# Kernel tuning notes

Hardware: AMD Instinct MI355X
Metric: run time of the kernel (lower is better)

The kernel has to match this reference:

```python
import jax, jax.numpy as jnp
import numpy as np

L = 2          # MPblock_layers
H = 64         # hidden_channels
B, N, E = 1, 50000, 800000


def setup_inputs() -> dict:
    key = jax.random.key(0)
    ks = jax.random.split(key, 12)
    s = 0.05
    return {
        "x": jax.random.normal(ks[0], (B, N, H), jnp.float32),
        "edge_attr": jax.random.normal(ks[1], (B, E, H), jnp.float32),
        "edge_index": jax.random.randint(ks[2], (2, E), 0, N, jnp.int64 if jax.config.jax_enable_x64 else jnp.int32),
        # per-layer stacked MLP params: edge MLP (3H->H->H), node MLP (2H->H->H)
        "edge_w1": jax.random.normal(ks[3], (L, 3 * H, H), jnp.float32) * s,
        "edge_b1": jnp.zeros((L, H), jnp.float32),
        "edge_w2": jax.random.normal(ks[4], (L, H, H), jnp.float32) * s,
        "edge_b2": jnp.zeros((L, H), jnp.float32),
        "node_w1": jax.random.normal(ks[5], (L, 2 * H, H), jnp.float32) * s,
        "node_b1": jnp.zeros((L, H), jnp.float32),
        "node_w2": jax.random.normal(ks[6], (L, H, H), jnp.float32) * s,
        "node_b2": jnp.zeros((L, H), jnp.float32),
    }


def reference(x, edge_attr, edge_index,
              edge_w1, edge_b1, edge_w2, edge_b2,
              node_w1, node_b1, node_w2, node_b2):
    src = edge_index[0]
    dest = edge_index[1]
    n_nodes = x.shape[1]
    for l in range(L):
        # EdgeModel: cat([edge_attr, x[src], x[dest]]) -> MLP
        cat_e = jnp.concatenate([edge_attr, x[:, src], x[:, dest]], axis=2)  # [B,E,3H]
        h = jax.nn.silu(jnp.einsum('bef,fh->beh', cat_e, edge_w1[l]) + edge_b1[l])
        edge_attr = jnp.einsum('beh,hk->bek', h, edge_w2[l]) + edge_b2[l]      # [B,E,H]
        # NodeModel: scatter_add over dest, cat with x, MLP
        agg = jnp.zeros((x.shape[0], n_nodes, edge_attr.shape[2]), x.dtype).at[:, dest].add(edge_attr)
        cat_n = jnp.concatenate([x, agg], axis=2)                              # [B,N,2H]
        h = jax.nn.silu(jnp.einsum('bnf,fh->bnh', cat_n, node_w1[l]) + node_b1[l])
        x = jnp.einsum('bnh,hk->bnk', h, node_w2[l]) + node_b2[l]              # [B,N,H]
    return (x, edge_attr)
```

## Files before the change

### kernel.cpp

```cpp
#include <hip/hip_runtime.h>

typedef __attribute__((ext_vector_type(8))) _Float16 f16x8;
typedef __attribute__((ext_vector_type(4))) _Float16 f16x4;
typedef __attribute__((ext_vector_type(4))) float f32x4;

#define PWS 72

__device__ __forceinline__ float silu_f(float v) {
    return v * (1.0f / (1.0f + __expf(-v)));
}

struct WDesc { const float* W; _Float16* out; int K; };
struct WPack { WDesc d[8]; };

__global__ __launch_bounds__(256) void conv_weights(WPack p) {
    WDesc wd = p.d[blockIdx.y];
    int total = wd.K * 64;
    int i = blockIdx.x * 256 + threadIdx.x;
    if (i >= total) return;
    int j  = i & 7;
    int l  = (i >> 3) & 63;
    int tn = i >> 9;
    int t  = tn >> 2, nf = tn & 3;
    int k  = t * 32 + (l >> 4) * 8 + j;
    int c  = nf * 16 + (l & 15);
    wd.out[i] = (_Float16)wd.W[k * 64 + c];
}

template <bool IN16, bool OUT16>
__global__ __launch_bounds__(256, 8) void gnn_edge_mfma(
    const float* __restrict__ x,
    const float* __restrict__ ea_in,
    const _Float16* __restrict__ ea_in16,
    float* __restrict__ ea_out,
    _Float16* __restrict__ ea_out16,
    const int* __restrict__ src_idx,
    const int* __restrict__ dst_idx,
    const _Float16* __restrict__ w1f,
    const float* __restrict__ b1,
    const _Float16* __restrict__ w2f,
    const float* __restrict__ b2,
    float* __restrict__ agg,
    int E)
{
    __shared__ __align__(16) _Float16 sA[64][PWS];

    const int t    = threadIdx.x;
    const int lane = t & 63;
    const int w    = t >> 6;
    const int col  = lane & 15;
    const int g    = lane >> 4;
    const int ko   = g * 8;
    const long base = (long)blockIdx.x * 64;

    long er0 = base + w * 16 + col;
    if (er0 >= E) er0 = E - 1;
    const int di = dst_idx[er0];

    f16x4  ea16v[4];
    float4 ea4[4];
    float4 sx4[4], dx4[4];
#pragma unroll
    for (int it = 0; it < 4; ++it) {
        long er = base + w * 16 + it * 4 + g;
        if (er >= E) er = E - 1;
        if constexpr (IN16) ea16v[it] = *(const f16x4*)(ea_in16 + er * 64 + col * 4);
        else                ea4[it]   = *(const float4*)(ea_in   + er * 64 + col * 4);
        sx4[it] = *(const float4*)(x + (long)src_idx[er] * 64 + col * 4);
        dx4[it] = *(const float4*)(x + (long)dst_idx[er] * 64 + col * 4);
    }

    f32x4 acc[4];
#pragma unroll
    for (int nf = 0; nf < 4; ++nf) {
        float bv = b1[nf * 16 + col];
        acc[nf] = (f32x4){bv, bv, bv, bv};
    }

    const int arow = w * 16 + col;

#define MFMA_L1(s3)                                                             \
    _Pragma("unroll")                                                           \
    for (int tt = 0; tt < 2; ++tt) {                                            \
        int k0 = tt * 32 + ko;                                                  \
        f16x8 af = *(const f16x8*)&sA[arow][k0];                                \
        int tg = (s3) * 2 + tt;                                                 \
        _Pragma("unroll")                                                       \
        for (int nf = 0; nf < 4; ++nf) {                                        \
            f16x8 bf = *(const f16x8*)(w1f + (size_t)((tg*4+nf)*64+lane)*8);    \
            acc[nf] = __builtin_amdgcn_mfma_f32_16x16x32_f16(af, bf, acc[nf], 0, 0, 0); \
        }                                                                       \
    }

#pragma unroll
    for (int it = 0; it < 4; ++it) {
        int rg = w * 16 + it * 4 + g;
        f16x4 hv;
        if constexpr (IN16) {
            hv = ea16v[it];
        } else {
            hv[0] = (_Float16)ea4[it].x; hv[1] = (_Float16)ea4[it].y;
            hv[2] = (_Float16)ea4[it].z; hv[3] = (_Float16)ea4[it].w;
        }
        *(f16x4*)&sA[rg][col * 4] = hv;
    }
    MFMA_L1(0)

#pragma unroll
    for (int it = 0; it < 4; ++it) {
        int rg = w * 16 + it * 4 + g;
        f16x4 hv;
        hv[0] = (_Float16)sx4[it].x; hv[1] = (_Float16)sx4[it].y;
        hv[2] = (_Float16)sx4[it].z; hv[3] = (_Float16)sx4[it].w;
        *(f16x4*)&sA[rg][col * 4] = hv;
    }
    MFMA_L1(1)

#pragma unroll
    for (int it = 0; it < 4; ++it) {
        int rg = w * 16 + it * 4 + g;
        f16x4 hv;
        hv[0] = (_Float16)dx4[it].x; hv[1] = (_Float16)dx4[it].y;
        hv[2] = (_Float16)dx4[it].z; hv[3] = (_Float16)dx4[it].w;
        *(f16x4*)&sA[rg][col * 4] = hv;
    }
    MFMA_L1(2)
#undef MFMA_L1

#pragma unroll
    for (int nf = 0; nf < 4; ++nf)
#pragma unroll
        for (int rg = 0; rg < 4; ++rg) {
            int row = w * 16 + g * 4 + rg;
            sA[row][nf * 16 + col] = (_Float16)silu_f(acc[nf][rg]);
        }

    f32x4 out[4];
#pragma unroll
    for (int nf = 0; nf < 4; ++nf) {
        float bv = b2[nf * 16 + col];
        out[nf] = (f32x4){bv, bv, bv, bv};
    }
#pragma unroll
    for (int tt = 0; tt < 2; ++tt) {
        int k0 = tt * 32 + ko;
        f16x8 af = *(const f16x8*)&sA[arow][k0];
#pragma unroll
        for (int nf = 0; nf < 4; ++nf) {
            f16x8 bf = *(const f16x8*)(w2f + (size_t)((tt * 4 + nf) * 64 + lane) * 8);
            out[nf] = __builtin_amdgcn_mfma_f32_16x16x32_f16(af, bf, out[nf], 0, 0, 0);
        }
    }

    const int rbase = w * 16 + g * 4;
#pragma unroll
    for (int rg = 0; rg < 4; ++rg) {
        long row = base + rbase + rg;
        if (row < E) {
            int drow = __shfl(di, g * 4 + rg);
            float* ap = agg + (long)drow * 64;
#pragma unroll
            for (int nf = 0; nf < 4; ++nf) {
                if constexpr (OUT16)
                    ea_out16[row * 64 + nf * 16 + col] = (_Float16)out[nf][rg];
                else
                    ea_out[row * 64 + nf * 16 + col] = out[nf][rg];
                atomicAdd(&ap[nf * 16 + col], out[nf][rg]);
            }
        }
    }
}

__global__ __launch_bounds__(256, 8) void gnn_node_mfma(
    const float* __restrict__ x_in,
    const float* __restrict__ aggp,
    float* __restrict__ x_out,
    const _Float16* __restrict__ w1f,
    const float* __restrict__ b1,
    const _Float16* __restrict__ w2f,
    const float* __restrict__ b2, int N)
{
    __shared__ __align__(16) _Float16 sA[64][PWS];

    const int t    = threadIdx.x;
    const int lane = t & 63;
    const int w    = t >> 6;
    const int col  = lane & 15;
    const int g    = lane >> 4;
    const int ko   = g * 8;
    const long base = (long)blockIdx.x * 64;

    long nr = base + w * 16 + col;
    if (nr >= N) nr = N - 1;
    const float* px = x_in + nr * 64 + ko;
    const float* pa = aggp + nr * 64 + ko;

    float4 v0 = *(const float4*)(px);
    float4 v1 = *(const float4*)(px + 4);
    float4 v2 = *(const float4*)(px + 32);
    float4 v3 = *(const float4*)(px + 36);
    float4 v4 = *(const float4*)(pa);
    float4 v5 = *(const float4*)(pa + 4);
    float4 v6 = *(const float4*)(pa + 32);
    float4 v7 = *(const float4*)(pa + 36);

    f32x4 acc[4];
#pragma unroll
    for (int nf = 0; nf < 4; ++nf) {
        float bv = b1[nf * 16 + col];
        acc[nf] = (f32x4){bv, bv, bv, bv};
    }

#define QTR(m, A, B)                                                            \
    {                                                                           \
        f16x8 af;                                                               \
        af[0] = (_Float16)A.x; af[1] = (_Float16)A.y;                           \
        af[2] = (_Float16)A.z; af[3] = (_Float16)A.w;                           \
        af[4] = (_Float16)B.x; af[5] = (_Float16)B.y;                           \
        af[6] = (_Float16)B.z; af[7] = (_Float16)B.w;                           \
        _Pragma("unroll")                                                       \
        for (int nf = 0; nf < 4; ++nf) {                                        \
            f16x8 bf = *(const f16x8*)(w1f + (size_t)(((m)*4+nf)*64+lane)*8);   \
            acc[nf] = __builtin_amdgcn_mfma_f32_16x16x32_f16(af, bf, acc[nf], 0, 0, 0); \
        }                                                                       \
    }
    QTR(0, v0, v1)  QTR(1, v2, v3)
    QTR(2, v4, v5)  QTR(3, v6, v7)
#undef QTR

#pragma unroll
    for (int nf = 0; nf < 4; ++nf)
#pragma unroll
        for (int rg = 0; rg < 4; ++rg) {
            int row = w * 16 + g * 4 + rg;
            sA[row][nf * 16 + col] = (_Float16)silu_f(acc[nf][rg]);
        }

    f32x4 out[4];
#pragma unroll
    for (int nf = 0; nf < 4; ++nf) {
        float bv = b2[nf * 16 + col];
        out[nf] = (f32x4){bv, bv, bv, bv};
    }
    const int arow = w * 16 + col;
#pragma unroll
    for (int tt = 0; tt < 2; ++tt) {
        int k0 = tt * 32 + ko;
        f16x8 af = *(const f16x8*)&sA[arow][k0];
#pragma unroll
        for (int nf = 0; nf < 4; ++nf) {
            f16x8 bf = *(const f16x8*)(w2f + (size_t)((tt * 4 + nf) * 64 + lane) * 8);
            out[nf] = __builtin_amdgcn_mfma_f32_16x16x32_f16(af, bf, out[nf], 0, 0, 0);
        }
    }

    const int rbase = w * 16 + g * 4;
#pragma unroll
    for (int rg = 0; rg < 4; ++rg) {
        long row = base + rbase + rg;
        if (row < N) {
            float* op = x_out + row * 64;
#pragma unroll
            for (int nf = 0; nf < 4; ++nf)
                op[nf * 16 + col] = out[nf][rg];
        }
    }
}

extern "C" void kernel_launch(void* const* d_in, const int* in_sizes, int n_in,
                              void* d_out, int out_size, void* d_ws, size_t ws_size,
                              hipStream_t stream) {
    const int H = 64;
    const int N = in_sizes[0] / H;
    const int E = in_sizes[1] / H;

    const float* x0  = (const float*)d_in[0];
    const float* ea0 = (const float*)d_in[1];
    const int*   ei  = (const int*)d_in[2];
    const float* ew1 = (const float*)d_in[3];
    const float* eb1 = (const float*)d_in[4];
    const float* ew2 = (const float*)d_in[5];
    const float* eb2 = (const float*)d_in[6];
    const float* nw1 = (const float*)d_in[7];
    const float* nb1 = (const float*)d_in[8];
    const float* nw2 = (const float*)d_in[9];
    const float* nb2 = (const float*)d_in[10];

    float* outX = (float*)d_out;
    float* outE = outX + (size_t)N * H;

    const size_t aggBytes = (size_t)N * H * sizeof(float);
    const size_t wElems   = 2 * ((size_t)(192 + 64 + 128 + 64) * 64);
    const size_t eaHBytes = (size_t)E * H * sizeof(_Float16);

    float* agg      = (float*)d_ws;
    _Float16* wbase = (_Float16*)((char*)d_ws + aggBytes);
    char* eaH_raw   = (char*)(wbase + wElems);
    eaH_raw = (char*)(((uintptr_t)eaH_raw + 15) & ~(uintptr_t)15);
    _Float16* eaH   = (_Float16*)eaH_raw;

    const bool useF16 = ((char*)eaH + eaHBytes) <= ((char*)d_ws + ws_size);

    const int* srcI = ei;
    const int* dstI = ei + E;

    WPack pack;
    size_t off = 0;
    _Float16* EW1[2]; _Float16* EW2[2]; _Float16* NW1[2]; _Float16* NW2[2];
    for (int l = 0; l < 2; ++l) {
        EW1[l] = wbase + off; off += 192 * 64;
        EW2[l] = wbase + off; off += 64 * 64;
        NW1[l] = wbase + off; off += 128 * 64;
        NW2[l] = wbase + off; off += 64 * 64;
        pack.d[l * 4 + 0] = {ew1 + (size_t)l * 192 * 64, EW1[l], 192};
        pack.d[l * 4 + 1] = {ew2 + (size_t)l * 64 * 64,  EW2[l], 64};
        pack.d[l * 4 + 2] = {nw1 + (size_t)l * 128 * 64, NW1[l], 128};
        pack.d[l * 4 + 3] = {nw2 + (size_t)l * 64 * 64,  NW2[l], 64};
    }
    conv_weights<<<dim3(48, 8), 256, 0, stream>>>(pack);

    const int egrid = (E + 63) / 64;
    const int ngrid = (N + 63) / 64;

    for (int l = 0; l < 2; ++l) {
        const float* xin = (l == 0) ? x0 : outX;
        (void)hipMemsetAsync(agg, 0, aggBytes, stream);
        if (useF16) {
            if (l == 0) {
                gnn_edge_mfma<false, true><<<egrid, 256, 0, stream>>>(
                    xin, ea0, nullptr, nullptr, eaH, srcI, dstI,
                    EW1[l], eb1 + l * H, EW2[l], eb2 + l * H, agg, E);
            } else {
                gnn_edge_mfma<true, false><<<egrid, 256, 0, stream>>>(
                    xin, nullptr, eaH, outE, nullptr, srcI, dstI,
                    EW1[l], eb1 + l * H, EW2[l], eb2 + l * H, agg, E);
            }
        } else {
            const float* eain = (l == 0) ? ea0 : outE;
            gnn_edge_mfma<false, false><<<egrid, 256, 0, stream>>>(
                xin, eain, nullptr, outE, nullptr, srcI, dstI,
                EW1[l], eb1 + l * H, EW2[l], eb2 + l * H, agg, E);
        }
        gnn_node_mfma<<<ngrid, 256, 0, stream>>>(
            xin, agg, outX,
            NW1[l], nb1 + l * H,
            NW2[l], nb2 + l * H,
            N);
    }
}
```

Baseline: 540.3 us.

## Sort edges by destination into CSR and replace atomic scatter with segmented reduction

Builds a destination-sorted CSR each call (histogram, single-block scan, atomic scatter) and runs the edge MLP in sorted order, writing fp16 edge outputs contiguously. A per-node segmented-sum kernel then replaces the float atomic scatter-add and the agg memset. The final layer also scatters fp32 results back to the original edge order. This adds sorting kernels, a serial 1024-thread scan and extra index traffic, and the edge_attr gather in layer one becomes a permuted read.

```diff
diff --git a/kernel.cpp b/kernel.cpp
--- a/kernel.cpp
+++ b/kernel.cpp
@@ -25,6 +25,223 @@
     int k  = t * 32 + (l >> 4) * 8 + j;
     int c  = nf * 16 + (l & 15);
     wd.out[i] = (_Float16)wd.W[k * 64 + c];
+}
+
+__global__ __launch_bounds__(256) void hist_kernel(const int* __restrict__ dst,
+                                                   int* __restrict__ counts, int E) {
+    int e = blockIdx.x * 256 + threadIdx.x;
+    if (e < E) atomicAdd(&counts[dst[e]], 1);
+}
+
+__global__ __launch_bounds__(1024) void scan_kernel(int* __restrict__ counts,
+                                                    int* __restrict__ row_ptr,
+                                                    int N, int E) {
+    __shared__ int part[1024];
+    int t = threadIdx.x;
+    int per = (N + 1023) >> 10;
+    int s = t * per, en = min(s + per, N);
+    int sum = 0;
+    for (int i = s; i < en; ++i) sum += counts[i];
+    part[t] = sum;
+    __syncthreads();
+    for (int off = 1; off < 1024; off <<= 1) {
+        int v = (t >= off) ? part[t - off] : 0;
+        __syncthreads();
+        part[t] += v;
+        __syncthreads();
+    }
+    int run = (t == 0) ? 0 : part[t - 1];
+    for (int i = s; i < en; ++i) {
+        int c = counts[i];
+        row_ptr[i] = run;
+        counts[i] = run;
+        run += c;
+    }
+    if (t == 1023) row_ptr[N] = E;
+}
+
+__global__ __launch_bounds__(256) void scatter_kernel(
+    const int* __restrict__ src, const int* __restrict__ dst,
+    int* __restrict__ cursor,
+    int* __restrict__ csr_eid, int* __restrict__ srcS, int* __restrict__ dstS,
+    int E) {
+    int e = blockIdx.x * 256 + threadIdx.x;
+    if (e < E) {
+        int d = dst[e];
+        int pos = atomicAdd(&cursor[d], 1);
+        csr_eid[pos] = e;
+        srcS[pos] = src[e];
+        dstS[pos] = d;
+    }
+}
+
+template <bool IN16, bool FINAL>
+__global__ __launch_bounds__(256, 8) void gnn_edge_sorted(
+    const float* __restrict__ x,
+    const float* __restrict__ ea0,
+    _Float16* __restrict__ ea_mid,
+    float* __restrict__ ea_out,
+    const int* __restrict__ csr_eid,
+    const int* __restrict__ srcS,
+    const int* __restrict__ dstS,
+    const _Float16* __restrict__ w1f,
+    const float* __restrict__ b1,
+    const _Float16* __restrict__ w2f,
+    const float* __restrict__ b2,
+    int E)
+{
+    __shared__ __align__(16) _Float16 sA[64][PWS];
+
+    const int t    = threadIdx.x;
+    const int lane = t & 63;
+    const int w    = t >> 6;
+    const int col  = lane & 15;
+    const int g    = lane >> 4;
+    const int ko   = g * 8;
+    const long base = (long)blockIdx.x * 64;
+
+    long p0 = base + w * 16 + col;
+    if (p0 >= E) p0 = E - 1;
+    int ei0 = 0;
+    if constexpr (FINAL) ei0 = csr_eid[p0];
+
+    f16x4  ea16v[4];
+    float4 ea4[4];
+    float4 sx4[4], dx4[4];
+#pragma unroll
+    for (int it = 0; it < 4; ++it) {
+        long p = base + w * 16 + it * 4 + g;
+        if (p >= E) p = E - 1;
+        int ss = srcS[p];
+        int ds = dstS[p];
+        if constexpr (IN16) {
+            ea16v[it] = *(const f16x4*)(ea_mid + p * 64 + col * 4);
+        } else {
+            int eid = csr_eid[p];
+            ea4[it] = *(const float4*)(ea0 + (long)eid * 64 + col * 4);
+        }
+        sx4[it] = *(const float4*)(x + (long)ss * 64 + col * 4);
+        dx4[it] = *(const float4*)(x + (long)ds * 64 + col * 4);
+    }
+
+    f32x4 acc[4];
+#pragma unroll
+    for (int nf = 0; nf < 4; ++nf) {
+        float bv = b1[nf * 16 + col];
+        acc[nf] = (f32x4){bv, bv, bv, bv};
+    }
+
+    const int arow = w * 16 + col;
+
+#define MFMA_L1(s3)                                                             \
+    _Pragma("unroll")                                                           \
+    for (int tt = 0; tt < 2; ++tt) {                                            \
+        int k0 = tt * 32 + ko;                                                  \
+        f16x8 af = *(const f16x8*)&sA[arow][k0];                                \
+        int tg = (s3) * 2 + tt;                                                 \
+        _Pragma("unroll")                                                       \
+        for (int nf = 0; nf < 4; ++nf) {                                        \
+            f16x8 bf = *(const f16x8*)(w1f + (size_t)((tg*4+nf)*64+lane)*8);    \
+            acc[nf] = __builtin_amdgcn_mfma_f32_16x16x32_f16(af, bf, acc[nf], 0, 0, 0); \
+        }                                                                       \
+    }
+
+#pragma unroll
+    for (int it = 0; it < 4; ++it) {
+        int rg = w * 16 + it * 4 + g;
+        f16x4 hv;
+        if constexpr (IN16) {
+            hv = ea16v[it];
+        } else {
+            hv[0] = (_Float16)ea4[it].x; hv[1] = (_Float16)ea4[it].y;
+            hv[2] = (_Float16)ea4[it].z; hv[3] = (_Float16)ea4[it].w;
+        }
+        *(f16x4*)&sA[rg][col * 4] = hv;
+    }
+    MFMA_L1(0)
+
+#pragma unroll
+    for (int it = 0; it < 4; ++it) {
+        int rg = w * 16 + it * 4 + g;
+        f16x4 hv;
+        hv[0] = (_Float16)sx4[it].x; hv[1] = (_Float16)sx4[it].y;
+        hv[2] = (_Float16)sx4[it].z; hv[3] = (_Float16)sx4[it].w;
+        *(f16x4*)&sA[rg][col * 4] = hv;
+    }
+    MFMA_L1(1)
+
+#pragma unroll
+    for (int it = 0; it < 4; ++it) {
+        int rg = w * 16 + it * 4 + g;
+        f16x4 hv;
+        hv[0] = (_Float16)dx4[it].x; hv[1] = (_Float16)dx4[it].y;
+        hv[2] = (_Float16)dx4[it].z; hv[3] = (_Float16)dx4[it].w;
+        *(f16x4*)&sA[rg][col * 4] = hv;
+    }
+    MFMA_L1(2)
+#undef MFMA_L1
+
+#pragma unroll
+    for (int nf = 0; nf < 4; ++nf)
+#pragma unroll
+        for (int rg = 0; rg < 4; ++rg) {
+            int row = w * 16 + g * 4 + rg;
+            sA[row][nf * 16 + col] = (_Float16)silu_f(acc[nf][rg]);
+        }
+
+    f32x4 out[4];
+#pragma unroll
+    for (int nf = 0; nf < 4; ++nf) {
+        float bv = b2[nf * 16 + col];
+        out[nf] = (f32x4){bv, bv, bv, bv};
+    }
+#pragma unroll
+    for (int tt = 0; tt < 2; ++tt) {
+        int k0 = tt * 32 + ko;
+        f16x8 af = *(const f16x8*)&sA[arow][k0];
+#pragma unroll
+        for (int nf = 0; nf < 4; ++nf) {
+            f16x8 bf = *(const f16x8*)(w2f + (size_t)((tt * 4 + nf) * 64 + lane) * 8);
+            out[nf] = __builtin_amdgcn_mfma_f32_16x16x32_f16(af, bf, out[nf], 0, 0, 0);
+        }
+    }
+
+    const int rbase = w * 16 + g * 4;
+#pragma unroll
+    for (int rg = 0; rg < 4; ++rg) {
+        long p = base + rbase + rg;
+        if (p < E) {
+#pragma unroll
+            for (int nf = 0; nf < 4; ++nf)
+                ea_mid[p * 64 + nf * 16 + col] = (_Float16)out[nf][rg];
+            if constexpr (FINAL) {
+                int eid = __shfl(ei0, g * 4 + rg);
+                float* op = ea_out + (long)eid * 64;
+#pragma unroll
+                for (int nf = 0; nf < 4; ++nf)
+                    op[nf * 16 + col] = out[nf][rg];
+            }
+        }
+    }
+}
+
+__global__ __launch_bounds__(256) void agg_seg(
+    const _Float16* __restrict__ ea_mid,
+    const int* __restrict__ row_ptr,
+    float* __restrict__ agg, int N)
+{
+    int t = threadIdx.x;
+    long n = (long)blockIdx.x * 16 + (t >> 4);
+    int q = t & 15;
+    if (n >= N) return;
+    int pe0 = row_ptr[n], pe1 = row_ptr[n + 1];
+    float a0 = 0.f, a1 = 0.f, a2 = 0.f, a3 = 0.f;
+    for (int p = pe0; p < pe1; ++p) {
+        f16x4 v = *(const f16x4*)(ea_mid + (long)p * 64 + q * 4);
+        a0 += (float)v[0]; a1 += (float)v[1];
+        a2 += (float)v[2]; a3 += (float)v[3];
+    }
+    *(float4*)(agg + n * 64 + q * 4) = make_float4(a0, a1, a2, a3);
 }
 
 template <bool IN16, bool OUT16>
@@ -76,7 +293,6 @@
         float bv = b1[nf * 16 + col];
         acc[nf] = (f32x4){bv, bv, bv, bv};
     }
-
     const int arow = w * 16 + col;
 
 #define MFMA_L1(s3)                                                             \
@@ -105,7 +321,6 @@
         *(f16x4*)&sA[rg][col * 4] = hv;
     }
     MFMA_L1(0)
-
 #pragma unroll
     for (int it = 0; it < 4; ++it) {
         int rg = w * 16 + it * 4 + g;
@@ -115,7 +330,6 @@
         *(f16x4*)&sA[rg][col * 4] = hv;
     }
     MFMA_L1(1)
-
 #pragma unroll
     for (int it = 0; it < 4; ++it) {
         int rg = w * 16 + it * 4 + g;
@@ -298,8 +512,14 @@
     char* eaH_raw   = (char*)(wbase + wElems);
     eaH_raw = (char*)(((uintptr_t)eaH_raw + 15) & ~(uintptr_t)15);
     _Float16* eaH   = (_Float16*)eaH_raw;
-
-    const bool useF16 = ((char*)eaH + eaHBytes) <= ((char*)d_ws + ws_size);
+    int* counts     = (int*)(((uintptr_t)((char*)eaH + eaHBytes) + 15) & ~(uintptr_t)15);
+    int* row_ptr    = counts + N;
+    int* csr_eid    = row_ptr + N + 1;
+    int* srcS       = csr_eid + E;
+    int* dstS       = srcS + E;
+
+    const bool sortedOK = ((char*)(dstS + E)) <= ((char*)d_ws + ws_size);
+    const bool f16OK    = ((char*)eaH + eaHBytes) <= ((char*)d_ws + ws_size);
 
     const int* srcI = ei;
     const int* dstI = ei + E;
@@ -321,30 +541,50 @@
 
     const int egrid = (E + 63) / 64;
     const int ngrid = (N + 63) / 64;
-
-    for (int l = 0; l < 2; ++l) {
-        const float* xin = (l == 0) ? x0 : outX;
-        (void)hipMemsetAsync(agg, 0, aggBytes, stream);
-        if (useF16) {
-            if (l == 0) {
-                gnn_edge_mfma<false, true><<<egrid, 256, 0, stream>>>(
-                    xin, ea0, nullptr, nullptr, eaH, srcI, dstI,
-                    EW1[l], eb1 + l * H, EW2[l], eb2 + l * H, agg, E);
+    const int agrid = (N + 15) / 16;
+
+    if (sortedOK) {
+        (void)hipMemsetAsync(counts, 0, (size_t)N * sizeof(int), stream);
+        hist_kernel<<<(E + 255) / 256, 256, 0, stream>>>(dstI, counts, E);
+        scan_kernel<<<1, 1024, 0, stream>>>(counts, row_ptr, N, E);
+        scatter_kernel<<<(E + 255) / 256, 256, 0, stream>>>(
+            srcI, dstI, counts, csr_eid, srcS, dstS, E);
+
+        gnn_edge_sorted<false, false><<<egrid, 256, 0, stream>>>(
+            x0, ea0, eaH, nullptr, csr_eid, srcS, dstS,
+            EW1[0], eb1, EW2[0], eb2, E);
+        agg_seg<<<agrid, 256, 0, stream>>>(eaH, row_ptr, agg, N);
+        gnn_node_mfma<<<ngrid, 256, 0, stream>>>(
+            x0, agg, outX, NW1[0], nb1, NW2[0], nb2, N);
+
+        gnn_edge_sorted<true, true><<<egrid, 256, 0, stream>>>(
+            outX, nullptr, eaH, outE, csr_eid, srcS, dstS,
+            EW1[1], eb1 + H, EW2[1], eb2 + H, E);
+        agg_seg<<<agrid, 256, 0, stream>>>(eaH, row_ptr, agg, N);
+        gnn_node_mfma<<<ngrid, 256, 0, stream>>>(
+            outX, agg, outX, NW1[1], nb1 + H, NW2[1], nb2 + H, N);
+    } else {
+        for (int l = 0; l < 2; ++l) {
+            const float* xin = (l == 0) ? x0 : outX;
+            (void)hipMemsetAsync(agg, 0, aggBytes, stream);
+            if (f16OK) {
+                if (l == 0)
+                    gnn_edge_mfma<false, true><<<egrid, 256, 0, stream>>>(
+                        xin, ea0, nullptr, nullptr, eaH, srcI, dstI,
+                        EW1[l], eb1 + l * H, EW2[l], eb2 + l * H, agg, E);
+                else
+                    gnn_edge_mfma<true, false><<<egrid, 256, 0, stream>>>(
+                        xin, nullptr, eaH, outE, nullptr, srcI, dstI,
+                        EW1[l], eb1 + l * H, EW2[l], eb2 + l * H, agg, E);
             } else {
-                gnn_edge_mfma<true, false><<<egrid, 256, 0, stream>>>(
-                    xin, nullptr, eaH, outE, nullptr, srcI, dstI,
+                const float* eain = (l == 0) ? ea0 : outE;
+                gnn_edge_mfma<false, false><<<egrid, 256, 0, stream>>>(
+                    xin, eain, nullptr, outE, nullptr, srcI, dstI,
                     EW1[l], eb1 + l * H, EW2[l], eb2 + l * H, agg, E);
             }
-        } else {
-            const float* eain = (l == 0) ? ea0 : outE;
-            gnn_edge_mfma<false, false><<<egrid, 256, 0, stream>>>(
-                xin, eain, nullptr, outE, nullptr, srcI, dstI,
-                EW1[l], eb1 + l * H, EW2[l], eb2 + l * H, agg, E);
-        }
-        gnn_node_mfma<<<ngrid, 256, 0, stream>>>(
-            xin, agg, outX,
-            NW1[l], nb1 + l * H,
-            NW2[l], nb2 + l * H,
-            N);
-    }
-}
+            gnn_node_mfma<<<ngrid, 256, 0, stream>>>(
+                xin, agg, outX,
+                NW1[l], nb1 + l * H, NW2[l], nb2 + l * H, N);
+        }
+    }
+}
```

Result: slower. 591.9 us (+9.5%).
